# Performance work log

Measured on AMD Instinct MI355X. Metric: run time of the kernel, lower is better.

Reference implementation:

```python
import jax, jax.numpy as jnp
import numpy as np

N = 50000      # nodes
E = 800000     # edges (avg degree 16)
F_IN = 32      # node_feat_dim
D = 128        # hidden_dim
L = 4          # n_layers
H = 8          # n_heads
DK = D // H    # 16
NB = 5         # n_bands
NS = 5         # n_stages
DFF = 4 * D    # ffn hidden


def setup_inputs() -> dict:
    key = jax.random.key(0)
    ks = jax.random.split(key, 24)
    s = 0.02
    inp = {}
    # forward args
    inp['x'] = jax.random.normal(ks[0], (N, F_IN), jnp.float32)
    inp['edge_index'] = jax.random.randint(ks[1], (2, E), 0, N)
    inp['edge_attr'] = jax.random.uniform(ks[2], (E,), jnp.float32)
    inp['band_ids'] = jax.random.randint(ks[3], (E,), 0, NB)
    inp['stage_ids'] = jax.random.randint(ks[4], (N,), 0, NS)
    # learned params (dropout in eval mode -> identity)
    inp['stage_emb'] = jax.random.normal(ks[5], (NS, D), jnp.float32) * s
    inp['in_w'] = jax.random.normal(ks[6], (F_IN, D), jnp.float32) * s
    inp['in_b'] = jnp.zeros((D,), jnp.float32)
    inp['Wq'] = jax.random.normal(ks[7], (L, D, D), jnp.float32) * s
    inp['Wk'] = jax.random.normal(ks[8], (L, D, D), jnp.float32) * s
    inp['Wv'] = jax.random.normal(ks[9], (L, D, D), jnp.float32) * s
    inp['Wo'] = jax.random.normal(ks[10], (L, D, D), jnp.float32) * s
    inp['Wo_b'] = jnp.zeros((L, D), jnp.float32)
    inp['band_bias'] = jax.random.normal(ks[11], (L, NB, H), jnp.float32) * s
    inp['ln1_g'] = jnp.ones((L, D), jnp.float32)
    inp['ln1_b'] = jnp.zeros((L, D), jnp.float32)
    inp['ffn_w1'] = jax.random.normal(ks[12], (L, D, DFF), jnp.float32) * s
    inp['ffn_b1'] = jnp.zeros((L, DFF), jnp.float32)
    inp['ffn_w2'] = jax.random.normal(ks[13], (L, DFF, D), jnp.float32) * s
    inp['ffn_b2'] = jnp.zeros((L, D), jnp.float32)
    inp['ln2_g'] = jnp.ones((L, D), jnp.float32)
    inp['ln2_b'] = jnp.zeros((L, D), jnp.float32)
    inp['out_w'] = jax.random.normal(ks[14], (D, D), jnp.float32) * s
    inp['out_b'] = jnp.zeros((D,), jnp.float32)
    return inp


def _layer_norm(x, g, b, eps=1e-5):
    m = x.mean(-1, keepdims=True)
    v = ((x - m) ** 2).mean(-1, keepdims=True)
    return (x - m) * jax.lax.rsqrt(v + eps) * g + b


def reference(x, edge_index, edge_attr, band_ids, stage_ids, stage_emb,
              in_w, in_b, Wq, Wk, Wv, Wo, Wo_b, band_bias,
              ln1_g, ln1_b, ffn_w1, ffn_b1, ffn_w2, ffn_b2,
              ln2_g, ln2_b, out_w, out_b):
    n = x.shape[0]
    src = edge_index[0]  # message sources (j)
    dst = edge_index[1]  # message targets (i) -> softmax / aggregation index
    scale = 1.0 / np.sqrt(DK).astype(np.float32)

    h = x @ in_w + in_b + stage_emb[stage_ids]  # (N, D)

    for l in range(L):
        Q = (h @ Wq[l]).reshape(n, H, DK)
        K = (h @ Wk[l]).reshape(n, H, DK)
        V = (h @ Wv[l]).reshape(n, H, DK)
        # edge-gather dot-product attention logits + band bias, (E, H)
        attn = jnp.einsum('ehd,ehd->eh', Q[dst], K[src]) * scale
        attn = (attn + band_bias[l][band_ids]) * edge_attr[:, None]
        # segment softmax over edges sharing the same destination node
        mx = jax.ops.segment_max(attn, dst, num_segments=n)  # (N, H)
        ex = jnp.exp(attn - mx[dst])
        sm = jax.ops.segment_sum(ex, dst, num_segments=n)
        a = ex / (sm[dst] + 1e-16)  # (E, H)
        # weighted scatter-add of V_j into destination nodes
        agg = jax.ops.segment_sum(a[:, :, None] * V[src], dst, num_segments=n)
        o = agg.reshape(n, D) @ Wo[l] + Wo_b[l]
        h = _layer_norm(o + h, ln1_g[l], ln1_b[l])  # residual (in_dim == out_dim)
        ff = jax.nn.gelu(h @ ffn_w1[l] + ffn_b1[l], approximate=False) @ ffn_w2[l] + ffn_b2[l]
        h = _layer_norm(h + ff, ln2_g[l], ln2_b[l])

    return h @ out_w + out_b
```

## Files before the change

kernel.cpp:

```cpp
#include <hip/hip_runtime.h>
#include <math.h>

constexpr int N_   = 50000;
constexpr int E_   = 800000;
constexpr int FIN_ = 32;
constexpr int D_   = 128;
constexpr int H_   = 8;
constexpr int NB_  = 5;
constexpr int L_   = 4;
constexpr int DFF_ = 512;

typedef __attribute__((ext_vector_type(8))) short short8;
typedef __attribute__((ext_vector_type(4))) short short4v;
typedef __attribute__((ext_vector_type(4))) float f32x4;
typedef __attribute__((ext_vector_type(2))) float f32x2;

__device__ __forceinline__ short f2bf(float f){
  unsigned u = __float_as_uint(f);
  unsigned r = (u + 0x7FFFu + ((u >> 16) & 1u)) >> 16;
  return (short)r;
}
__device__ __forceinline__ float bf2f(short v){
  return __uint_as_float(((unsigned)(unsigned short)v) << 16);
}
__device__ __forceinline__ float bflo(unsigned u){ return __uint_as_float(u << 16); }
__device__ __forceinline__ float bfhi(unsigned u){ return __uint_as_float(u & 0xffff0000u); }

__device__ __forceinline__ unsigned char f2fp8(float x){
  int p = __builtin_amdgcn_cvt_pk_fp8_f32(x, x, 0, false);
  return (unsigned char)(p & 0xFF);
}

__device__ __forceinline__ float gelu_f(float x){
  float xs = x * 0.70710678118654752f;
  float ax = fabsf(xs);
  float t  = __builtin_amdgcn_rcpf(1.0f + 0.3275911f*ax);
  float y  = t*(0.254829592f + t*(-0.284496736f + t*(1.421413741f +
             t*(-1.453152027f + t*1.061405429f))));
  float e  = exp2f(-ax*ax*1.4426950408889634f);
  float er = 1.0f - y*e;
  er = __uint_as_float((__float_as_uint(er) & 0x7fffffffu) |
                       (__float_as_uint(xs) & 0x80000000u));
  return 0.5f*x*(1.0f + er);
}

__device__ __forceinline__ size_t pfidx(int n, int k, int K){
  return ((size_t)(n >> 4)*(2*K) + (size_t)(k >> 3)*16 + (n & 15))*8 + (k & 7);
}

__global__ __launch_bounds__(256)
void conv_weights(const float* __restrict__ Wq, const float* __restrict__ Wk,
                  const float* __restrict__ Wv, const float* __restrict__ Wo,
                  const float* __restrict__ w1, const float* __restrict__ w2,
                  const float* __restrict__ ow,
                  short* __restrict__ wqkvt, short* __restrict__ wot,
                  short* __restrict__ w1t, short* __restrict__ w2t,
                  short* __restrict__ owt){
  int idx = blockIdx.x * blockDim.x + threadIdx.x;
  if (idx < 3*L_*16384){
    int m = idx / (L_*16384);
    int r = idx % (L_*16384);
    int l = r / 16384, e = r % 16384;
    int k = e >> 7, n = e & 127;
    const float* src = (m == 0) ? Wq : ((m == 1) ? Wk : Wv);
    wqkvt[(size_t)(l*3 + m)*16384 + pfidx(n, k, 128)] = f2bf(src[(size_t)l*16384 + e]);
    return;
  }
  idx -= 3*L_*16384;
  if (idx < L_*16384){
    int l = idx / 16384, e = idx % 16384, k = e >> 7, n = e & 127;
    wot[(size_t)l*16384 + pfidx(n, k, 128)] = f2bf(Wo[idx]);
    return;
  }
  idx -= L_*16384;
  if (idx < L_*D_*DFF_){
    int l = idx / 65536, e = idx % 65536;
    int k = e >> 9, n = e & 511;
    w1t[(size_t)l*65536 + pfidx(n, k, 128)] = f2bf(w1[idx]);
    return;
  }
  idx -= L_*D_*DFF_;
  if (idx < L_*DFF_*D_){
    int l = idx / 65536, e = idx % 65536;
    int k = e >> 7, n = e & 127;
    w2t[(size_t)l*65536 + pfidx(n, k, 512)] = f2bf(w2[idx]);
    return;
  }
  idx -= L_*DFF_*D_;
  if (idx < 16384){
    int k = idx >> 7, n = idx & 127;
    owt[pfidx(n, k, 128)] = f2bf(ow[idx]);
  }
}

__global__ __launch_bounds__(256)
void input_proj(const float* __restrict__ x, const float* __restrict__ in_w,
                const float* __restrict__ in_b, const float* __restrict__ se,
                const int* __restrict__ sid, short* __restrict__ hb){
  int sub = threadIdx.x >> 7, d = threadIdx.x & 127;
  int i = blockIdx.x*2 + sub;
  __shared__ float xs[2][FIN_];
  if (d < FIN_) xs[sub][d] = x[(size_t)i*FIN_ + d];
  __syncthreads();
  float acc = in_b[d] + se[(size_t)sid[i]*D_ + d];
  #pragma unroll 8
  for (int k=0;k<FIN_;k++) acc += xs[sub][k]*in_w[k*D_+d];
  hb[(size_t)i*D_+d] = f2bf(acc);
}

__global__ void k_deg(const int* __restrict__ dst, const int* __restrict__ src,
                      const int* __restrict__ band,
                      int* __restrict__ deg, int* __restrict__ pk){
  int e = blockIdx.x*blockDim.x + threadIdx.x;
  if (e < E_){
    atomicAdd(&deg[dst[e]], 1);
    pk[e] = src[e] | (band[e] << 16);
  }
}

__global__ __launch_bounds__(1024)
void k_scan1(const int* __restrict__ deg, int* __restrict__ rowptr,
             int* __restrict__ bsum){
  __shared__ int sm[1024];
  int b = blockIdx.x, tid = threadIdx.x;
  int i = b*1024 + tid;
  int v = (i < N_) ? deg[i] : 0;
  sm[tid] = v; __syncthreads();
  for (int off=1; off<1024; off<<=1){
    int t = (tid>=off) ? sm[tid-off] : 0;
    __syncthreads();
    sm[tid] += t;
    __syncthreads();
  }
  if (i < N_) rowptr[i+1] = sm[tid];
  if (tid == 1023) bsum[b] = sm[1023];
}

__global__ void k_scan2(int* __restrict__ bsum, int nb){
  int tid = threadIdx.x;
  int v = (tid < nb) ? bsum[tid] : 0;
  for (int off=1; off<64; off<<=1){
    int t = __shfl_up(v, off, 64);
    if (tid >= off) v += t;
  }
  if (tid < nb) bsum[tid] = v;
}

__global__ void k_scan3(int* __restrict__ rowptr, const int* __restrict__ bsum){
  int i = blockIdx.x*blockDim.x + threadIdx.x;
  if (i == 0) rowptr[0] = 0;
  if (i < N_){
    int b = i >> 10;
    if (b > 0) rowptr[i+1] += bsum[b-1];
  }
}

__global__ void k_scatter(const int* __restrict__ dst, const int* __restrict__ rowptr,
                          int* __restrict__ fill, int* __restrict__ eord){
  int e = blockIdx.x*blockDim.x + threadIdx.x;
  if (e < E_){
    int d = dst[e];
    int pos = rowptr[d] + atomicAdd(&fill[d], 1);
    eord[pos] = e;
  }
}

__global__ void k_sortseg(const int* __restrict__ rowptr, int* __restrict__ eord){
  int i = blockIdx.x*blockDim.x + threadIdx.x;
  if (i >= N_) return;
  int b = rowptr[i], t = rowptr[i+1];
  for (int p = b+1; p < t; p++){
    int v = eord[p];
    int q = p-1;
    while (q >= b && eord[q] > v){ eord[q+1] = eord[q]; q--; }
    eord[q+1] = v;
  }
}

__global__ void k_emeta(const int* __restrict__ eord, const int* __restrict__ pk,
                        const float* __restrict__ eattr, int2* __restrict__ em){
  int p = blockIdx.x*blockDim.x + threadIdx.x;
  if (p < E_){
    int e = eord[p];
    em[p] = make_int2(pk[e], __float_as_int(eattr[e]));
  }
}

template<int EPI>
__global__ __launch_bounds__(512, 2)
void gemm128_direct(const short* __restrict__ A, const short* __restrict__ Wt,
                    const float* __restrict__ bias,
                    float* Cf, short* Yb, unsigned char* KV8, int M, long wstride){
  const int tid = threadIdx.x;
  const int by  = blockIdx.y;
  Wt += (size_t)by * wstride;
  const short8* W8 = (const short8*)Wt;
  const int m0 = blockIdx.x * 128;
  const int lane = tid & 63, w = tid >> 6;
  const int wr = w >> 2, wc = w & 3;
  const int lrow = lane & 15, lgrp = lane >> 4;
  f32x4 acc[4][2];
  #pragma unroll
  for (int r=0;r<4;r++){ acc[r][0] = {0.f,0.f,0.f,0.f}; acc[r][1] = {0.f,0.f,0.f,0.f}; }
  int rowA[4];
  #pragma unroll
  for (int r=0;r<4;r++){
    int rr = m0 + wr*64 + r*16 + lrow;
    rowA[r] = (rr < M) ? rr : (M-1);
  }
  #pragma unroll
  for (int kk = 0; kk < 4; kk++){
    const int koff = kk*32 + lgrp*8;
    short8 af[4], bfr[2];
    #pragma unroll
    for (int r = 0; r < 4; r++)
      af[r] = *(const short8*)(A + (size_t)rowA[r]*128 + koff);
    #pragma unroll
    for (int c = 0; c < 2; c++)
      bfr[c] = W8[(size_t)(wc*2 + c)*256 + kk*64 + lane];
    #pragma unroll
    for (int r = 0; r < 4; r++)
      #pragma unroll
      for (int c = 0; c < 2; c++)
        acc[r][c] = __builtin_amdgcn_mfma_f32_16x16x32_bf16(af[r], bfr[c], acc[r][c], 0, 0, 0);
  }
  #pragma unroll
  for (int r = 0; r < 4; r++){
    #pragma unroll
    for (int c = 0; c < 2; c++){
      int col = wc*32 + c*16 + lrow;
      float bv = (EPI == 3) ? bias[col] : 0.f;
      #pragma unroll
      for (int v = 0; v < 4; v++){
        int row = m0 + wr*64 + r*16 + lgrp*4 + v;
        if (row < M){
          float o = acc[r][c][v] + bv;
          if (EPI == 3) Cf[(size_t)row*128 + col] = o;
          else if (by == 0) Yb[(size_t)row*128 + col] = f2bf(o);
          else KV8[(size_t)row*256 + (by-1)*128 + col] = f2fp8(o);
        }
      }
    }
  }
}

__global__ __launch_bounds__(512, 4)
void gemm_ln_direct(const short* __restrict__ A, const short* __restrict__ Wt,
                    const float* __restrict__ bias, const short* __restrict__ Rb,
                    short* __restrict__ Yb, int M,
                    const float* __restrict__ g_ln, const float* __restrict__ b_ln){
  __shared__ float rsum[4][64];
  __shared__ float rsq[4][64];
  const int tid = threadIdx.x;
  const int m0 = blockIdx.x * 64;
  const int lane = tid & 63, w = tid >> 6;
  const int wr = w >> 2, wc = w & 3;
  const int lrow = lane & 15, lgrp = lane >> 4;
  const short8* W8 = (const short8*)Wt;
  f32x4 acc[2][2];
  #pragma unroll
  for (int r=0;r<2;r++){ acc[r][0] = {0.f,0.f,0.f,0.f}; acc[r][1] = {0.f,0.f,0.f,0.f}; }
  int rowA[2];
  #pragma unroll
  for (int r=0;r<2;r++){
    int rr = m0 + wr*32 + r*16 + lrow;
    rowA[r] = (rr < M) ? rr : (M-1);
  }
  #pragma unroll
  for (int kk = 0; kk < 4; kk++){
    const int koff = kk*32 + lgrp*8;
    short8 af[2], bfr[2];
    #pragma unroll
    for (int r = 0; r < 2; r++)
      af[r] = *(const short8*)(A + (size_t)rowA[r]*128 + koff);
    #pragma unroll
    for (int c = 0; c < 2; c++)
      bfr[c] = W8[(size_t)(wc*2 + c)*256 + kk*64 + lane];
    #pragma unroll
    for (int r = 0; r < 2; r++)
      #pragma unroll
      for (int c = 0; c < 2; c++)
        acc[r][c] = __builtin_amdgcn_mfma_f32_16x16x32_bf16(af[r], bfr[c], acc[r][c], 0, 0, 0);
  }
  float o[2][2][4];
  float ps[2][4], pq[2][4];
  #pragma unroll
  for (int r=0;r<2;r++)
    #pragma unroll
    for (int v=0;v<4;v++){ ps[r][v]=0.f; pq[r][v]=0.f; }
  #pragma unroll
  for (int r = 0; r < 2; r++){
    #pragma unroll
    for (int c = 0; c < 2; c++){
      int col = wc*32 + c*16 + lrow;
      float bv = bias[col];
      #pragma unroll
      for (int v = 0; v < 4; v++){
        int grow = m0 + wr*32 + r*16 + lgrp*4 + v;
        int gr = (grow < M) ? grow : (M-1);
        float oo = acc[r][c][v] + bv + bf2f(Rb[(size_t)gr*128 + col]);
        o[r][c][v] = oo;
        ps[r][v] += oo;
        pq[r][v] += oo*oo;
      }
    }
  }
  #pragma unroll
  for (int r = 0; r < 2; r++)
    #pragma unroll
    for (int v = 0; v < 4; v++){
      #pragma unroll
      for (int off = 1; off < 16; off <<= 1){
        ps[r][v] += __shfl_xor(ps[r][v], off, 16);
        pq[r][v] += __shfl_xor(pq[r][v], off, 16);
      }
    }
  if (lrow == 0){
    #pragma unroll
    for (int r = 0; r < 2; r++)
      #pragma unroll
      for (int v = 0; v < 4; v++){
        int row = wr*32 + r*16 + lgrp*4 + v;
        rsum[wc][row] = ps[r][v];
        rsq[wc][row]  = pq[r][v];
      }
  }
  __syncthreads();
  #pragma unroll
  for (int r = 0; r < 2; r++){
    float gv[2], bv2[2];
    #pragma unroll
    for (int c = 0; c < 2; c++){
      int col = wc*32 + c*16 + lrow;
      gv[c] = g_ln[col]; bv2[c] = b_ln[col];
    }
    #pragma unroll
    for (int v = 0; v < 4; v++){
      int row = wr*32 + r*16 + lgrp*4 + v;
      int grow = m0 + row;
      float s = (rsum[0][row]+rsum[1][row]) + (rsum[2][row]+rsum[3][row]);
      float q = (rsq[0][row]+rsq[1][row]) + (rsq[2][row]+rsq[3][row]);
      float mean = s * (1.f/128.f);
      float var  = q * (1.f/128.f) - mean*mean;
      float rstd = rsqrtf(var + 1e-5f);
      if (grow < M){
        #pragma unroll
        for (int c = 0; c < 2; c++){
          int col = wc*32 + c*16 + lrow;
          float y = (o[r][c][v] - mean)*rstd*gv[c] + bv2[c];
          Yb[(size_t)grow*128 + col] = f2bf(y);
        }
      }
    }
  }
}

__global__ __launch_bounds__(512, 4)
void ffn_fused(short* __restrict__ hb,
               const short* __restrict__ w1t, const float* __restrict__ b1,
               const short* __restrict__ w2t, const float* __restrict__ b2,
               const float* __restrict__ g2, const float* __restrict__ bl2,
               int M){
  __shared__ char smem[16384];
  __shared__ float rsum[4][64];
  __shared__ float rsq[4][64];
  const int tid = threadIdx.x;
  const int m0 = blockIdx.x * 64;
  const int lane = tid & 63, w = tid >> 6;
  const int lrow = lane & 15, lgrp = lane >> 4;
  const int wr = w >> 2, wc = w & 3;
  const short8* W18 = (const short8*)w1t;
  const short8* W28 = (const short8*)w2t;
  f32x4 acc2[2][2];
  #pragma unroll
  for (int r=0;r<2;r++){ acc2[r][0] = {0.f,0.f,0.f,0.f}; acc2[r][1] = {0.f,0.f,0.f,0.f}; }
  int rowA[2];
  #pragma unroll
  for (int r=0;r<2;r++){
    int rr = m0 + wr*32 + r*16 + lrow;
    rowA[r] = (rr < M) ? rr : (M-1);
  }
  #pragma unroll
  for (int chunk = 0; chunk < 4; chunk++){
    f32x4 acc1[2][2];
    #pragma unroll
    for (int r=0;r<2;r++){ acc1[r][0] = {0.f,0.f,0.f,0.f}; acc1[r][1] = {0.f,0.f,0.f,0.f}; }
    #pragma unroll
    for (int kk = 0; kk < 4; kk++){
      const int koff = kk*32 + lgrp*8;
      short8 af[2], bfr[2];
      #pragma unroll
      for (int r = 0; r < 2; r++)
        af[r] = *(const short8*)(hb + (size_t)rowA[r]*128 + koff);
      #pragma unroll
      for (int c = 0; c < 2; c++){
        int nb = chunk*8 + wc*2 + c;
        bfr[c] = W18[(size_t)nb*256 + kk*64 + lane];
      }
      #pragma unroll
      for (int r = 0; r < 2; r++)
        #pragma unroll
        for (int c = 0; c < 2; c++)
          acc1[r][c] = __builtin_amdgcn_mfma_f32_16x16x32_bf16(af[r], bfr[c], acc1[r][c], 0, 0, 0);
    }
    __syncthreads();
    #pragma unroll
    for (int r = 0; r < 2; r++){
      #pragma unroll
      for (int c = 0; c < 2; c++){
        int lc = wc*32 + c*16 + lrow;
        float bv = b1[chunk*128 + lc];
        #pragma unroll
        for (int v = 0; v < 4; v++){
          int row = wr*32 + r*16 + lgrp*4 + v;
          float g = gelu_f(acc1[r][c][v] + bv);
          int off = row*256 + lc*2;
          *(short*)(smem + (off ^ ((row & 7) << 4))) = f2bf(g);
        }
      }
    }
    __syncthreads();
    #pragma unroll
    for (int kk2 = 0; kk2 < 4; kk2++){
      short8 ah[2], bh[2];
      #pragma unroll
      for (int r = 0; r < 2; r++){
        int row = wr*32 + r*16 + lrow;
        ah[r] = *(const short8*)(smem + ((row*256 + kk2*64 + lgrp*16) ^ ((row & 7) << 4)));
      }
      #pragma unroll
      for (int c = 0; c < 2; c++){
        int nb = wc*2 + c;
        bh[c] = W28[(size_t)nb*1024 + chunk*256 + kk2*64 + lane];
      }
      #pragma unroll
      for (int r = 0; r < 2; r++)
        #pragma unroll
        for (int c = 0; c < 2; c++)
          acc2[r][c] = __builtin_amdgcn_mfma_f32_16x16x32_bf16(ah[r], bh[c], acc2[r][c], 0, 0, 0);
    }
  }
  float o[2][2][4];
  float ps[2][4], pq[2][4];
  #pragma unroll
  for (int r=0;r<2;r++)
    #pragma unroll
    for (int v=0;v<4;v++){ ps[r][v]=0.f; pq[r][v]=0.f; }
  #pragma unroll
  for (int r = 0; r < 2; r++){
    #pragma unroll
    for (int c = 0; c < 2; c++){
      int col = wc*32 + c*16 + lrow;
      float bv = b2[col];
      #pragma unroll
      for (int v = 0; v < 4; v++){
        int grow = m0 + wr*32 + r*16 + lgrp*4 + v;
        int gr = (grow < M) ? grow : (M-1);
        float oo = acc2[r][c][v] + bv + bf2f(hb[(size_t)gr*128 + col]);
        o[r][c][v] = oo;
        ps[r][v] += oo;
        pq[r][v] += oo*oo;
      }
    }
  }
  #pragma unroll
  for (int r = 0; r < 2; r++)
    #pragma unroll
    for (int v = 0; v < 4; v++){
      #pragma unroll
      for (int off = 1; off < 16; off <<= 1){
        ps[r][v] += __shfl_xor(ps[r][v], off, 16);
        pq[r][v] += __shfl_xor(pq[r][v], off, 16);
      }
    }
  if (lrow == 0){
    #pragma unroll
    for (int r = 0; r < 2; r++)
      #pragma unroll
      for (int v = 0; v < 4; v++){
        int row = wr*32 + r*16 + lgrp*4 + v;
        rsum[wc][row] = ps[r][v];
        rsq[wc][row]  = pq[r][v];
      }
  }
  __syncthreads();
  #pragma unroll
  for (int r = 0; r < 2; r++){
    float gv[2], bv2[2];
    #pragma unroll
    for (int c = 0; c < 2; c++){
      int col = wc*32 + c*16 + lrow;
      gv[c] = g2[col]; bv2[c] = bl2[col];
    }
    #pragma unroll
    for (int v = 0; v < 4; v++){
      int row = wr*32 + r*16 + lgrp*4 + v;
      int grow = m0 + row;
      float s = (rsum[0][row]+rsum[1][row]) + (rsum[2][row]+rsum[3][row]);
      float q = (rsq[0][row]+rsq[1][row]) + (rsq[2][row]+rsq[3][row]);
      float mean = s * (1.f/128.f);
      float var  = q * (1.f/128.f) - mean*mean;
      float rstd = rsqrtf(var + 1e-5f);
      if (grow < M){
        #pragma unroll
        for (int c = 0; c < 2; c++){
          int col = wc*32 + c*16 + lrow;
          float y = (o[r][c][v] - mean)*rstd*gv[c] + bv2[c];
          hb[(size_t)grow*128 + col] = f2bf(y);
        }
      }
    }
  }
}

__global__ __launch_bounds__(256, 8)
void attn_fused(const short* __restrict__ Qb, const unsigned char* __restrict__ KV8,
                const int2* __restrict__ em,
                const int* __restrict__ rowptr,
                const float* __restrict__ bb_l, short* __restrict__ aggb){
  const int lane = threadIdx.x & 63;
  const int i = (blockIdx.x << 2) + (threadIdx.x >> 6);
  if (i >= N_) return;
  const int hh = lane >> 3;
  const unsigned qw = ((const unsigned*)Qb)[(size_t)i*64 + lane];
  const float q0 = bflo(qw), q1 = bfhi(qw);
  const int p0 = __builtin_amdgcn_readfirstlane(rowptr[i]);
  const int p1 = __builtin_amdgcn_readfirstlane(rowptr[i+1]);
  constexpr float L2E = 1.442695040888963f;
  float2 outv = {0.f, 0.f};
  if (p0 < p1){
    float s[4]; float2 acc[4];
    #pragma unroll
    for (int c=0;c<4;c++){ s[c]=0.f; acc[c].x=0.f; acc[c].y=0.f; }
    int sj[4], sjN[4];
    float bb[4], ea[4], bbN[4], eaN[4];
    int kw[4], vw[4], kwN[4], vwN[4];

    auto ldmeta = [&](int gb, int* SJ, float* BB, float* EA){
      #pragma unroll
      for (int c = 0; c < 4; c++){
        int idx = gb + c; idx = (idx < p1) ? idx : (p1 - 1);
        int2 m = em[idx];
        unsigned u = (unsigned)__builtin_amdgcn_readfirstlane(m.x);
        SJ[c] = (int)(u & 0xFFFFu);
        BB[c] = bb_l[(u >> 16)*H_ + hh];
        EA[c] = __uint_as_float((unsigned)__builtin_amdgcn_readfirstlane(m.y));
      }
    };

    ldmeta(p0, sj, bb, ea);
    #pragma unroll
    for (int c = 0; c < 4; c++){
      kw[c] = *(const unsigned short*)(KV8 + (size_t)sj[c]*256 + lane*2);
      vw[c] = *(const unsigned short*)(KV8 + (size_t)sj[c]*256 + 128 + lane*2);
    }
    ldmeta(p0 + 4, sjN, bbN, eaN);

    for (int base = p0; base < p1; base += 4){
      #pragma unroll
      for (int c = 0; c < 4; c++){
        kwN[c] = *(const unsigned short*)(KV8 + (size_t)sjN[c]*256 + lane*2);
        vwN[c] = *(const unsigned short*)(KV8 + (size_t)sjN[c]*256 + 128 + lane*2);
      }
      int sj2[4]; float bb2[4], ea2[4];
      ldmeta(base + 8, sj2, bb2, ea2);
      #pragma unroll
      for (int c = 0; c < 4; c++){
        f32x2 kf = __builtin_amdgcn_cvt_pk_f32_fp8(kw[c], false);
        float dot = q0*kf[0] + q1*kf[1];
        dot += __shfl_xor(dot, 1, 8);
        dot += __shfl_xor(dot, 2, 8);
        dot += __shfl_xor(dot, 4, 8);
        float logit = (dot*0.25f + bb[c]) * ea[c];
        logit = fminf(logit, 60.f);
        if (base + c >= p1) logit = -1.0e30f;
        float wgt = exp2f(logit * L2E);
        f32x2 vf = __builtin_amdgcn_cvt_pk_f32_fp8(vw[c], false);
        s[c]     += wgt;
        acc[c].x += wgt*vf[0];
        acc[c].y += wgt*vf[1];
      }
      #pragma unroll
      for (int c = 0; c < 4; c++){
        kw[c]=kwN[c]; vw[c]=vwN[c];
        sj[c]=sjN[c]; bb[c]=bbN[c]; ea[c]=eaN[c];
        sjN[c]=sj2[c]; bbN[c]=bb2[c]; eaN[c]=ea2[c];
      }
    }
    float S = (s[0]+s[1]) + (s[2]+s[3]);
    float Ax = (acc[0].x+acc[1].x) + (acc[2].x+acc[3].x);
    float Ay = (acc[0].y+acc[1].y) + (acc[2].y+acc[3].y);
    float inv = 1.0f / (S + 1e-16f);
    outv.x = Ax * inv;
    outv.y = Ay * inv;
  }
  unsigned lo = (unsigned)(unsigned short)f2bf(outv.x);
  unsigned hi = (unsigned)(unsigned short)f2bf(outv.y);
  ((unsigned*)aggb)[(size_t)i*64 + lane] = lo | (hi << 16);
}

extern "C" void kernel_launch(void* const* d_in, const int* in_sizes, int n_in,
                              void* d_out, int out_size, void* d_ws, size_t ws_size,
                              hipStream_t stream) {
  const float* x         = (const float*)d_in[0];
  const int*   edge_index= (const int*)  d_in[1];
  const float* edge_attr = (const float*)d_in[2];
  const int*   band_ids  = (const int*)  d_in[3];
  const int*   stage_ids = (const int*)  d_in[4];
  const float* stage_emb = (const float*)d_in[5];
  const float* in_w      = (const float*)d_in[6];
  const float* in_b      = (const float*)d_in[7];
  const float* Wq        = (const float*)d_in[8];
  const float* Wk        = (const float*)d_in[9];
  const float* Wv        = (const float*)d_in[10];
  const float* Wo        = (const float*)d_in[11];
  const float* Wo_b      = (const float*)d_in[12];
  const float* band_bias = (const float*)d_in[13];
  const float* ln1_g     = (const float*)d_in[14];
  const float* ln1_b     = (const float*)d_in[15];
  const float* ffn_w1    = (const float*)d_in[16];
  const float* ffn_b1    = (const float*)d_in[17];
  const float* ffn_w2    = (const float*)d_in[18];
  const float* ffn_b2    = (const float*)d_in[19];
  const float* ln2_g     = (const float*)d_in[20];
  const float* ln2_b     = (const float*)d_in[21];
  const float* out_w     = (const float*)d_in[22];
  const float* out_b     = (const float*)d_in[23];
  float* out = (float*)d_out;

  const size_t ND = (size_t)N_*D_;
  float* ws  = (float*)d_ws;
  short* hb   = (short*)ws;
  short* hbp  = (short*)(ws + ND/2);
  short* aggb = (short*)(ws + ND);
  short* qb   = (short*)(ws + 2*ND);
  unsigned char* kv8 = (unsigned char*)(ws + 2*ND + ND/2);
  short* wbuf = (short*)(ws + 3*ND + ND/2);
  short* wqkvt = wbuf;
  short* wot   = wbuf + 196608;
  short* w1t   = wbuf + 262144;
  short* w2t   = wbuf + 524288;
  short* owt   = wbuf + 786432;
  int*  ibase = (int*)(ws + 3*ND + ND/2 + 401408);
  int*  deg   = ibase;
  int*  fill  = ibase + N_;
  int*  rowptr= ibase + 2*N_;
  int*  eord  = ibase + 3*N_ + 1;
  int*  bsum  = ibase + 3*N_ + 1 + E_;
  int*  pk    = ibase + 3*N_ + 1 + E_ + 64;
  int2* em    = (int2*)(ibase + 3*N_ + 1 + 2*E_ + 64);

  const int* srcA = edge_index;
  const int* dstA = edge_index + E_;

  hipMemsetAsync(deg, 0, 2ull*N_*sizeof(int), stream);

  conv_weights<<<3136, 256, 0, stream>>>(Wq, Wk, Wv, Wo, ffn_w1, ffn_w2, out_w,
                                         wqkvt, wot, w1t, w2t, owt);
  input_proj<<<N_/2, 256, 0, stream>>>(x, in_w, in_b, stage_emb, stage_ids, hb);

  k_deg   <<<(E_+255)/256, 256, 0, stream>>>(dstA, srcA, band_ids, deg, pk);
  k_scan1 <<<49, 1024, 0, stream>>>(deg, rowptr, bsum);
  k_scan2 <<<1, 64, 0, stream>>>(bsum, 49);
  k_scan3 <<<(N_+255)/256, 256, 0, stream>>>(rowptr, bsum);
  k_scatter<<<(E_+255)/256, 256, 0, stream>>>(dstA, rowptr, fill, eord);
  k_sortseg<<<(N_+255)/256, 256, 0, stream>>>(rowptr, eord);
  k_emeta <<<(E_+255)/256, 256, 0, stream>>>(eord, pk, edge_attr, em);

  const int GB  = (N_ + 127) / 128;
  const int GB2 = (N_ + 63) / 64;
  const int AB  = (N_ + 3) / 4;

  for (int l = 0; l < L_; l++){
    gemm128_direct<4><<<dim3(GB,3), 512, 0, stream>>>(
        hb, wqkvt + (size_t)l*3*16384, nullptr, nullptr, qb, kv8, N_, 16384L);

    attn_fused<<<AB, 256, 0, stream>>>(qb, kv8, em, rowptr,
                                       band_bias + l*NB_*H_, aggb);

    gemm_ln_direct<<<GB2, 512, 0, stream>>>(
        aggb, wot + (size_t)l*16384, Wo_b + l*D_, hb, hb,
        N_, ln1_g + l*D_, ln1_b + l*D_);

    ffn_fused<<<GB2, 512, 0, stream>>>(
        hb, w1t + (size_t)l*65536, ffn_b1 + l*DFF_,
        w2t + (size_t)l*65536, ffn_b2 + l*D_,
        ln2_g + l*D_, ln2_b + l*D_, N_);
  }

  gemm128_direct<3><<<GB, 512, 0, stream>>>(
      hb, owt, out_b, out, nullptr, nullptr, N_, 0L);
}
```

Measured before the change: 798.4 us.

## Fuse output projection + LayerNorm1 into the FFN kernel via shared-memory tile

Merges the Wo projection with residual and LayerNorm kernel into the FFN kernel. The post-LN1 tile stays in shared memory as the FFN input and the second residual, instead of being written to and reread from global memory. This saves one kernel launch per layer and a global round trip of the hidden state. The cost is an extra 16KB of LDS per block, which could lower occupancy, plus an added barrier before the reuse of the reduction buffers.

```diff
diff --git a/kernel.cpp b/kernel.cpp
--- a/kernel.cpp
+++ b/kernel.cpp
@@ -245,10 +245,15 @@
 }
 
 __global__ __launch_bounds__(512, 4)
-void gemm_ln_direct(const short* __restrict__ A, const short* __restrict__ Wt,
-                    const float* __restrict__ bias, const short* __restrict__ Rb,
-                    short* __restrict__ Yb, int M,
-                    const float* __restrict__ g_ln, const float* __restrict__ b_ln){
+void wo_ffn_fused(const short* __restrict__ aggb, const short* __restrict__ wot,
+                  const float* __restrict__ wo_b, short* __restrict__ hb,
+                  const short* __restrict__ w1t, const float* __restrict__ b1,
+                  const short* __restrict__ w2t, const float* __restrict__ b2,
+                  const float* __restrict__ g1, const float* __restrict__ bl1,
+                  const float* __restrict__ g2, const float* __restrict__ bl2,
+                  int M){
+  __shared__ char ytile[16384];
+  __shared__ char hidb[16384];
   __shared__ float rsum[4][64];
   __shared__ float rsq[4][64];
   const int tid = threadIdx.x;
@@ -256,130 +261,111 @@
   const int lane = tid & 63, w = tid >> 6;
   const int wr = w >> 2, wc = w & 3;
   const int lrow = lane & 15, lgrp = lane >> 4;
-  const short8* W8 = (const short8*)Wt;
-  f32x4 acc[2][2];
-  #pragma unroll
-  for (int r=0;r<2;r++){ acc[r][0] = {0.f,0.f,0.f,0.f}; acc[r][1] = {0.f,0.f,0.f,0.f}; }
   int rowA[2];
   #pragma unroll
   for (int r=0;r<2;r++){
     int rr = m0 + wr*32 + r*16 + lrow;
     rowA[r] = (rr < M) ? rr : (M-1);
   }
-  #pragma unroll
-  for (int kk = 0; kk < 4; kk++){
-    const int koff = kk*32 + lgrp*8;
-    short8 af[2], bfr[2];
+
+  {
+    const short8* W8 = (const short8*)wot;
+    f32x4 acc[2][2];
+    #pragma unroll
+    for (int r=0;r<2;r++){ acc[r][0] = {0.f,0.f,0.f,0.f}; acc[r][1] = {0.f,0.f,0.f,0.f}; }
+    #pragma unroll
+    for (int kk = 0; kk < 4; kk++){
+      const int koff = kk*32 + lgrp*8;
+      short8 af[2], bfr[2];
+      #pragma unroll
+      for (int r = 0; r < 2; r++)
+        af[r] = *(const short8*)(aggb + (size_t)rowA[r]*128 + koff);
+      #pragma unroll
+      for (int c = 0; c < 2; c++)
+        bfr[c] = W8[(size_t)(wc*2 + c)*256 + kk*64 + lane];
+      #pragma unroll
+      for (int r = 0; r < 2; r++)
+        #pragma unroll
+        for (int c = 0; c < 2; c++)
+          acc[r][c] = __builtin_amdgcn_mfma_f32_16x16x32_bf16(af[r], bfr[c], acc[r][c], 0, 0, 0);
+    }
+    float o[2][2][4];
+    float ps[2][4], pq[2][4];
+    #pragma unroll
+    for (int r=0;r<2;r++)
+      #pragma unroll
+      for (int v=0;v<4;v++){ ps[r][v]=0.f; pq[r][v]=0.f; }
+    #pragma unroll
+    for (int r = 0; r < 2; r++){
+      #pragma unroll
+      for (int c = 0; c < 2; c++){
+        int col = wc*32 + c*16 + lrow;
+        float bv = wo_b[col];
+        #pragma unroll
+        for (int v = 0; v < 4; v++){
+          int grow = m0 + wr*32 + r*16 + lgrp*4 + v;
+          int gr = (grow < M) ? grow : (M-1);
+          float oo = acc[r][c][v] + bv + bf2f(hb[(size_t)gr*128 + col]);
+          o[r][c][v] = oo;
+          ps[r][v] += oo;
+          pq[r][v] += oo*oo;
+        }
+      }
+    }
     #pragma unroll
     for (int r = 0; r < 2; r++)
-      af[r] = *(const short8*)(A + (size_t)rowA[r]*128 + koff);
-    #pragma unroll
-    for (int c = 0; c < 2; c++)
-      bfr[c] = W8[(size_t)(wc*2 + c)*256 + kk*64 + lane];
-    #pragma unroll
-    for (int r = 0; r < 2; r++)
-      #pragma unroll
-      for (int c = 0; c < 2; c++)
-        acc[r][c] = __builtin_amdgcn_mfma_f32_16x16x32_bf16(af[r], bfr[c], acc[r][c], 0, 0, 0);
-  }
-  float o[2][2][4];
-  float ps[2][4], pq[2][4];
-  #pragma unroll
-  for (int r=0;r<2;r++)
-    #pragma unroll
-    for (int v=0;v<4;v++){ ps[r][v]=0.f; pq[r][v]=0.f; }
-  #pragma unroll
-  for (int r = 0; r < 2; r++){
-    #pragma unroll
-    for (int c = 0; c < 2; c++){
-      int col = wc*32 + c*16 + lrow;
-      float bv = bias[col];
       #pragma unroll
       for (int v = 0; v < 4; v++){
-        int grow = m0 + wr*32 + r*16 + lgrp*4 + v;
-        int gr = (grow < M) ? grow : (M-1);
-        float oo = acc[r][c][v] + bv + bf2f(Rb[(size_t)gr*128 + col]);
-        o[r][c][v] = oo;
-        ps[r][v] += oo;
-        pq[r][v] += oo*oo;
-      }
-    }
-  }
-  #pragma unroll
-  for (int r = 0; r < 2; r++)
-    #pragma unroll
-    for (int v = 0; v < 4; v++){
-      #pragma unroll
-      for (int off = 1; off < 16; off <<= 1){
-        ps[r][v] += __shfl_xor(ps[r][v], off, 16);
-        pq[r][v] += __shfl_xor(pq[r][v], off, 16);
-      }
-    }
-  if (lrow == 0){
-    #pragma unroll
-    for (int r = 0; r < 2; r++)
+        #pragma unroll
+        for (int off = 1; off < 16; off <<= 1){
+          ps[r][v] += __shfl_xor(ps[r][v], off, 16);
+          pq[r][v] += __shfl_xor(pq[r][v], off, 16);
+        }
+      }
+    if (lrow == 0){
+      #pragma unroll
+      for (int r = 0; r < 2; r++)
+        #pragma unroll
+        for (int v = 0; v < 4; v++){
+          int row = wr*32 + r*16 + lgrp*4 + v;
+          rsum[wc][row] = ps[r][v];
+          rsq[wc][row]  = pq[r][v];
+        }
+    }
+    __syncthreads();
+    #pragma unroll
+    for (int r = 0; r < 2; r++){
+      float gv[2], bv2[2];
+      #pragma unroll
+      for (int c = 0; c < 2; c++){
+        int col = wc*32 + c*16 + lrow;
+        gv[c] = g1[col]; bv2[c] = bl1[col];
+      }
       #pragma unroll
       for (int v = 0; v < 4; v++){
         int row = wr*32 + r*16 + lgrp*4 + v;
-        rsum[wc][row] = ps[r][v];
-        rsq[wc][row]  = pq[r][v];
-      }
-  }
-  __syncthreads();
-  #pragma unroll
-  for (int r = 0; r < 2; r++){
-    float gv[2], bv2[2];
-    #pragma unroll
-    for (int c = 0; c < 2; c++){
-      int col = wc*32 + c*16 + lrow;
-      gv[c] = g_ln[col]; bv2[c] = b_ln[col];
-    }
-    #pragma unroll
-    for (int v = 0; v < 4; v++){
-      int row = wr*32 + r*16 + lgrp*4 + v;
-      int grow = m0 + row;
-      float s = (rsum[0][row]+rsum[1][row]) + (rsum[2][row]+rsum[3][row]);
-      float q = (rsq[0][row]+rsq[1][row]) + (rsq[2][row]+rsq[3][row]);
-      float mean = s * (1.f/128.f);
-      float var  = q * (1.f/128.f) - mean*mean;
-      float rstd = rsqrtf(var + 1e-5f);
-      if (grow < M){
+        float s = (rsum[0][row]+rsum[1][row]) + (rsum[2][row]+rsum[3][row]);
+        float q = (rsq[0][row]+rsq[1][row]) + (rsq[2][row]+rsq[3][row]);
+        float mean = s * (1.f/128.f);
+        float var  = q * (1.f/128.f) - mean*mean;
+        float rstd = rsqrtf(var + 1e-5f);
         #pragma unroll
         for (int c = 0; c < 2; c++){
           int col = wc*32 + c*16 + lrow;
           float y = (o[r][c][v] - mean)*rstd*gv[c] + bv2[c];
-          Yb[(size_t)grow*128 + col] = f2bf(y);
-        }
-      }
-    }
-  }
-}
-
-__global__ __launch_bounds__(512, 4)
-void ffn_fused(short* __restrict__ hb,
-               const short* __restrict__ w1t, const float* __restrict__ b1,
-               const short* __restrict__ w2t, const float* __restrict__ b2,
-               const float* __restrict__ g2, const float* __restrict__ bl2,
-               int M){
-  __shared__ char smem[16384];
-  __shared__ float rsum[4][64];
-  __shared__ float rsq[4][64];
-  const int tid = threadIdx.x;
-  const int m0 = blockIdx.x * 64;
-  const int lane = tid & 63, w = tid >> 6;
-  const int lrow = lane & 15, lgrp = lane >> 4;
-  const int wr = w >> 2, wc = w & 3;
+          int off = row*256 + col*2;
+          *(short*)(ytile + (off ^ ((row & 7) << 4))) = f2bf(y);
+        }
+      }
+    }
+  }
+  __syncthreads();
+
   const short8* W18 = (const short8*)w1t;
   const short8* W28 = (const short8*)w2t;
   f32x4 acc2[2][2];
   #pragma unroll
   for (int r=0;r<2;r++){ acc2[r][0] = {0.f,0.f,0.f,0.f}; acc2[r][1] = {0.f,0.f,0.f,0.f}; }
-  int rowA[2];
-  #pragma unroll
-  for (int r=0;r<2;r++){
-    int rr = m0 + wr*32 + r*16 + lrow;
-    rowA[r] = (rr < M) ? rr : (M-1);
-  }
   #pragma unroll
   for (int chunk = 0; chunk < 4; chunk++){
     f32x4 acc1[2][2];
@@ -390,8 +376,10 @@
       const int koff = kk*32 + lgrp*8;
       short8 af[2], bfr[2];
       #pragma unroll
-      for (int r = 0; r < 2; r++)
-        af[r] = *(const short8*)(hb + (size_t)rowA[r]*128 + koff);
+      for (int r = 0; r < 2; r++){
+        int row = wr*32 + r*16 + lrow;
+        af[r] = *(const short8*)(ytile + ((row*256 + koff*2) ^ ((row & 7) << 4)));
+      }
       #pragma unroll
       for (int c = 0; c < 2; c++){
         int nb = chunk*8 + wc*2 + c;
@@ -415,7 +403,7 @@
           int row = wr*32 + r*16 + lgrp*4 + v;
           float g = gelu_f(acc1[r][c][v] + bv);
           int off = row*256 + lc*2;
-          *(short*)(smem + (off ^ ((row & 7) << 4))) = f2bf(g);
+          *(short*)(hidb + (off ^ ((row & 7) << 4))) = f2bf(g);
         }
       }
     }
@@ -426,7 +414,7 @@
       #pragma unroll
       for (int r = 0; r < 2; r++){
         int row = wr*32 + r*16 + lrow;
-        ah[r] = *(const short8*)(smem + ((row*256 + kk2*64 + lgrp*16) ^ ((row & 7) << 4)));
+        ah[r] = *(const short8*)(hidb + ((row*256 + kk2*64 + lgrp*16) ^ ((row & 7) << 4)));
       }
       #pragma unroll
       for (int c = 0; c < 2; c++){
@@ -440,73 +428,78 @@
           acc2[r][c] = __builtin_amdgcn_mfma_f32_16x16x32_bf16(ah[r], bh[c], acc2[r][c], 0, 0, 0);
     }
   }
-  float o[2][2][4];
-  float ps[2][4], pq[2][4];
-  #pragma unroll
-  for (int r=0;r<2;r++)
-    #pragma unroll
-    for (int v=0;v<4;v++){ ps[r][v]=0.f; pq[r][v]=0.f; }
-  #pragma unroll
-  for (int r = 0; r < 2; r++){
-    #pragma unroll
-    for (int c = 0; c < 2; c++){
-      int col = wc*32 + c*16 + lrow;
-      float bv = b2[col];
+
+  {
+    float o2[2][2][4];
+    float ps[2][4], pq[2][4];
+    #pragma unroll
+    for (int r=0;r<2;r++)
+      #pragma unroll
+      for (int v=0;v<4;v++){ ps[r][v]=0.f; pq[r][v]=0.f; }
+    #pragma unroll
+    for (int r = 0; r < 2; r++){
+      #pragma unroll
+      for (int c = 0; c < 2; c++){
+        int col = wc*32 + c*16 + lrow;
+        float bv = b2[col];
+        #pragma unroll
+        for (int v = 0; v < 4; v++){
+          int row = wr*32 + r*16 + lgrp*4 + v;
+          int off = row*256 + col*2;
+          float res = bf2f(*(const short*)(ytile + (off ^ ((row & 7) << 4))));
+          float oo = acc2[r][c][v] + bv + res;
+          o2[r][c][v] = oo;
+          ps[r][v] += oo;
+          pq[r][v] += oo*oo;
+        }
+      }
+    }
+    #pragma unroll
+    for (int r = 0; r < 2; r++)
       #pragma unroll
       for (int v = 0; v < 4; v++){
-        int grow = m0 + wr*32 + r*16 + lgrp*4 + v;
-        int gr = (grow < M) ? grow : (M-1);
-        float oo = acc2[r][c][v] + bv + bf2f(hb[(size_t)gr*128 + col]);
-        o[r][c][v] = oo;
-        ps[r][v] += oo;
-        pq[r][v] += oo*oo;
-      }
-    }
-  }
-  #pragma unroll
-  for (int r = 0; r < 2; r++)
-    #pragma unroll
-    for (int v = 0; v < 4; v++){
-      #pragma unroll
-      for (int off = 1; off < 16; off <<= 1){
-        ps[r][v] += __shfl_xor(ps[r][v], off, 16);
-        pq[r][v] += __shfl_xor(pq[r][v], off, 16);
-      }
-    }
-  if (lrow == 0){
-    #pragma unroll
-    for (int r = 0; r < 2; r++)
+        #pragma unroll
+        for (int off = 1; off < 16; off <<= 1){
+          ps[r][v] += __shfl_xor(ps[r][v], off, 16);
+          pq[r][v] += __shfl_xor(pq[r][v], off, 16);
+        }
+      }
+    __syncthreads();
+    if (lrow == 0){
+      #pragma unroll
+      for (int r = 0; r < 2; r++)
+        #pragma unroll
+        for (int v = 0; v < 4; v++){
+          int row = wr*32 + r*16 + lgrp*4 + v;
+          rsum[wc][row] = ps[r][v];
+          rsq[wc][row]  = pq[r][v];
+        }
+    }
+    __syncthreads();
+    #pragma unroll
+    for (int r = 0; r < 2; r++){
+      float gv[2], bv2[2];
+      #pragma unroll
+      for (int c = 0; c < 2; c++){
+        int col = wc*32 + c*16 + lrow;
+        gv[c] = g2[col]; bv2[c] = bl2[col];
+      }
       #pragma unroll
       for (int v = 0; v < 4; v++){
         int row = wr*32 + r*16 + lgrp*4 + v;
-        rsum[wc][row] = ps[r][v];
-        rsq[wc][row]  = pq[r][v];
-      }
-  }
-  __syncthreads();
-  #pragma unroll
-  for (int r = 0; r < 2; r++){
-    float gv[2], bv2[2];
-    #pragma unroll
-    for (int c = 0; c < 2; c++){
-      int col = wc*32 + c*16 + lrow;
-      gv[c] = g2[col]; bv2[c] = bl2[col];
-    }
-    #pragma unroll
-    for (int v = 0; v < 4; v++){
-      int row = wr*32 + r*16 + lgrp*4 + v;
-      int grow = m0 + row;
-      float s = (rsum[0][row]+rsum[1][row]) + (rsum[2][row]+rsum[3][row]);
-      float q = (rsq[0][row]+rsq[1][row]) + (rsq[2][row]+rsq[3][row]);
-      float mean = s * (1.f/128.f);
-      float var  = q * (1.f/128.f) - mean*mean;
-      float rstd = rsqrtf(var + 1e-5f);
-      if (grow < M){
-        #pragma unroll
-        for (int c = 0; c < 2; c++){
-          int col = wc*32 + c*16 + lrow;
-          float y = (o[r][c][v] - mean)*rstd*gv[c] + bv2[c];
-          hb[(size_t)grow*128 + col] = f2bf(y);
+        int grow = m0 + row;
+        float s = (rsum[0][row]+rsum[1][row]) + (rsum[2][row]+rsum[3][row]);
+        float q = (rsq[0][row]+rsq[1][row]) + (rsq[2][row]+rsq[3][row]);
+        float mean = s * (1.f/128.f);
+        float var  = q * (1.f/128.f) - mean*mean;
+        float rstd = rsqrtf(var + 1e-5f);
+        if (grow < M){
+          #pragma unroll
+          for (int c = 0; c < 2; c++){
+            int col = wc*32 + c*16 + lrow;
+            float y = (o2[r][c][v] - mean)*rstd*gv[c] + bv2[c];
+            hb[(size_t)grow*128 + col] = f2bf(y);
+          }
         }
       }
     }
@@ -631,7 +624,6 @@
   const size_t ND = (size_t)N_*D_;
   float* ws  = (float*)d_ws;
   short* hb   = (short*)ws;
-  short* hbp  = (short*)(ws + ND/2);
   short* aggb = (short*)(ws + ND);
   short* qb   = (short*)(ws + 2*ND);
   unsigned char* kv8 = (unsigned char*)(ws + 2*ND + ND/2);
@@ -678,14 +670,11 @@
     attn_fused<<<AB, 256, 0, stream>>>(qb, kv8, em, rowptr,
                                        band_bias + l*NB_*H_, aggb);
 
-    gemm_ln_direct<<<GB2, 512, 0, stream>>>(
-        aggb, wot + (size_t)l*16384, Wo_b + l*D_, hb, hb,
-        N_, ln1_g + l*D_, ln1_b + l*D_);
-
-    ffn_fused<<<GB2, 512, 0, stream>>>(
-        hb, w1t + (size_t)l*65536, ffn_b1 + l*DFF_,
+    wo_ffn_fused<<<GB2, 512, 0, stream>>>(
+        aggb, wot + (size_t)l*16384, Wo_b + l*D_, hb,
+        w1t + (size_t)l*65536, ffn_b1 + l*DFF_,
         w2t + (size_t)l*65536, ffn_b2 + l*D_,
-        ln2_g + l*D_, ln2_b + l*D_, N_);
+        ln1_g + l*D_, ln1_b + l*D_, ln2_g + l*D_, ln2_b + l*D_, N_);
   }
 
   gemm128_direct<3><<<GB, 512, 0, stream>>>(
```

After: 741.4 us. 1.08x faster.
